# Kernel tuning notes

Hardware: AMD Instinct MI355X
Metric: run time of the kernel (lower is better)

Reference implementation:

```python
import jax, jax.numpy as jnp
import numpy as np

EPS = 1e-5  # torch LayerNorm default eps
L2_EPS = 1e-12


def _l2norm(t, axis=-1):
    return t / jnp.sqrt(jnp.sum(t * t, axis=axis, keepdims=True) + L2_EPS)


def setup_inputs() -> dict:
    key = jax.random.key(0)
    k1, k2, k3 = jax.random.split(key, 3)
    b, n, d = 4, 2048, 1024
    h, e, cs = 8, 16, 2048
    x = jax.random.normal(k1, (b, n, d), dtype=jnp.float32)
    # xavier_normal_ on [h, d, e]: fan_in = d*e, fan_out = h*e
    std = float(np.sqrt(2.0 / (d * e + h * e)))
    rand_projs = jax.random.normal(k2, (h, d, e), dtype=jnp.float32) * std
    codebook = jax.random.normal(k3, (h, cs, e), dtype=jnp.float32)
    return {"x": x, "rand_projs": rand_projs, "codebook": codebook}


def reference(x, rand_projs, codebook):
    # LayerNorm over last dim, no affine
    mu = jnp.mean(x, axis=-1, keepdims=True)
    var = jnp.mean((x - mu) ** 2, axis=-1, keepdims=True)
    xn = (x - mu) / jnp.sqrt(var + EPS)
    # per-head random projection: [b,n,d] x [h,d,e] -> [b,n,h,e]
    proj = jnp.einsum('bnd,hde->bnhe', xn, rand_projs)
    # cosine-sim VQ per head: normalize both, argmax similarity
    q = _l2norm(proj, axis=-1)                 # [b,n,h,e]
    cb = _l2norm(codebook, axis=-1)            # [h,c,e]
    sim = jnp.einsum('bnhe,hce->bnhc', q, cb)  # [b,n,h,c]
    indices = jnp.argmax(sim, axis=-1)         # [b,n,h] int
    return indices
```

## Files before the change

kernel.cpp:

```cpp
#include <hip/hip_runtime.h>
#include <math.h>


typedef short bf16x8 __attribute__((ext_vector_type(8)));
typedef float f32x4 __attribute__((ext_vector_type(4)));

__device__ __forceinline__ void stage16(const float* g, float* lds_base) {
  __builtin_amdgcn_global_load_lds(
      (const __attribute__((address_space(1))) void*)g,
      (__attribute__((address_space(3))) void*)lds_base, 16, 0, 0);
}

__device__ __forceinline__ unsigned short f2bf(float f) {
  unsigned u = __builtin_bit_cast(unsigned, f);
  unsigned r = (u + 0x7FFFu + ((u >> 16) & 1u)) >> 16;
  return (unsigned short)r;
}
__device__ __forceinline__ float bf2f(unsigned short b) {
  return __builtin_bit_cast(float, (unsigned)b << 16);
}
__device__ __forceinline__ void split3(float v, unsigned short& h,
                                       unsigned short& m, unsigned short& l) {
  h = f2bf(v);
  float r = v - bf2f(h);
  m = f2bf(r);
  float r2 = r - bf2f(m);
  l = f2bf(r2);
}

__global__ __launch_bounds__(256) void k_cbnorm(const float* __restrict__ cb,
                                                unsigned short* __restrict__ cfrag) {
  int v = blockIdx.x * 256 + threadIdx.x;
  int h = v >> 11, c = v & 2047, tl = c >> 4, n = c & 15;
  const float4* p = (const float4*)(cb + (size_t)v * 16);
  float4 q0 = p[0], q1 = p[1], q2 = p[2], q3 = p[3];
  float f[16] = {q0.x,q0.y,q0.z,q0.w, q1.x,q1.y,q1.z,q1.w,
                 q2.x,q2.y,q2.z,q2.w, q3.x,q3.y,q3.z,q3.w};
  double s = 0.0;
#pragma unroll
  for (int i = 0; i < 16; ++i) s += (double)f[i] * (double)f[i];
  double inv = 1.0 / sqrt(s + 1e-12);
  __attribute__((aligned(16))) unsigned short vp[3][16];
#pragma unroll
  for (int i = 0; i < 16; ++i)
    split3((float)((double)f[i] * inv), vp[0][i], vp[1][i], vp[2][i]);
#pragma unroll
  for (int pp = 0; pp < 3; ++pp) {
    size_t base = ((((size_t)h * 128 + tl) * 3 + pp) * 16 + n) * 16;
    ((bf16x8*)(cfrag + base))[0] = ((bf16x8*)vp[pp])[0];
    ((bf16x8*)(cfrag + base))[1] = ((bf16x8*)vp[pp])[1];
  }
}

__global__ __launch_bounds__(256) void k_colsum(const float* __restrict__ W,
                                                float* __restrict__ cs) {
  __shared__ float red[16][17];
  int h = blockIdx.x;
  int e = threadIdx.x & 15, part = threadIdx.x >> 4;
  const float* base = W + h * 16384 + e;
  float s = 0.f;
  int d0 = part * 64;
  for (int i = 0; i < 64; ++i) s += base[(d0 + i) * 16];
  red[e][part] = s;
  __syncthreads();
  if (threadIdx.x < 16) {
    float t = 0.f;
#pragma unroll
    for (int p = 0; p < 16; ++p) t += red[threadIdx.x][p];
    cs[h * 16 + threadIdx.x] = t;
  }
}

__global__ __launch_bounds__(256) void k_wsplit(const float* __restrict__ W,
                                                unsigned short* __restrict__ wfrag) {
  int id = blockIdx.x * 256 + threadIdx.x;
  int o = id & 1, n = (id >> 1) & 15, c = (id >> 5) & 7, dg = id >> 8;
  __attribute__((aligned(16))) unsigned short vp[3][8];
#pragma unroll
  for (int j = 0; j < 8; ++j) {
    float v = W[c * 16384 + (dg * 16 + o * 8 + j) * 16 + n];
    split3(v, vp[0][j], vp[1][j], vp[2][j]);
  }
#pragma unroll
  for (int pp = 0; pp < 3; ++pp) {
    size_t base = ((((size_t)dg * 8 + c) * 3 + pp) * 16 + n) * 16 + o * 8;
    *(bf16x8*)(wfrag + base) = *(bf16x8*)vp[pp];
  }
}

__global__ __launch_bounds__(256) void k_proj(const float* __restrict__ x,
                                              const unsigned short* __restrict__ wfrag,
                                              const float* __restrict__ csum,
                                              unsigned short* __restrict__ ph,
                                              unsigned short* __restrict__ pm,
                                              unsigned short* __restrict__ pl) {
  __shared__ float sAcc[4][64][33];
  __shared__ float sPs[4][2][16];
  __shared__ float sMu[16];
  const int t = threadIdx.x;
  const int lane = t & 63, w = t >> 6;
  const int r0 = blockIdx.x * 16;
  const int q = lane >> 4, n16 = lane & 15, oct = q & 1;
  const bool qlt2 = (q < 2);
  const int p1 = qlt2 ? 0 : 1, p2 = qlt2 ? 1 : 0, p3 = qlt2 ? 2 : 0;
  const int row = r0 + n16;

  f32x4 acc[8];
#pragma unroll
  for (int h = 0; h < 8; ++h) acc[h] = (f32x4){0.f, 0.f, 0.f, 0.f};
  float ps = 0.f;

  for (int dg2 = 0; dg2 < 16; ++dg2) {
    const int dg = w * 16 + dg2;
    const int dq = dg * 16 + oct * 8;
    float4 xa = *(const float4*)(x + (size_t)row * 1024 + dq);
    float4 xb = *(const float4*)(x + (size_t)row * 1024 + dq + 4);
    float xf[8] = {xa.x, xa.y, xa.z, xa.w, xb.x, xb.y, xb.z, xb.w};
    ps += ((xf[0] + xf[1]) + (xf[2] + xf[3])) +
          ((xf[4] + xf[5]) + (xf[6] + xf[7]));
    __attribute__((aligned(16))) unsigned short s1[8], s3[8];
#pragma unroll
    for (int j = 0; j < 8; ++j) {
      unsigned short hh, mm, ll;
      split3(xf[j], hh, mm, ll);
      s1[j] = qlt2 ? hh : mm;
      s3[j] = qlt2 ? hh : ll;
    }
    bf16x8 a1 = *(bf16x8*)s1;
    bf16x8 a3 = *(bf16x8*)s3;
#pragma unroll
    for (int hh = 0; hh < 8; ++hh) {
      size_t b0 = (((size_t)(dg * 8 + hh) * 3) * 16 + n16) * 16 + oct * 8;
      bf16x8 b1 = *(const bf16x8*)(wfrag + b0 + p1 * 256);
      bf16x8 b2 = *(const bf16x8*)(wfrag + b0 + p2 * 256);
      bf16x8 b3 = *(const bf16x8*)(wfrag + b0 + p3 * 256);
      acc[hh] = __builtin_amdgcn_mfma_f32_16x16x32_bf16(a1, b1, acc[hh], 0, 0, 0);
      acc[hh] = __builtin_amdgcn_mfma_f32_16x16x32_bf16(a1, b2, acc[hh], 0, 0, 0);
      acc[hh] = __builtin_amdgcn_mfma_f32_16x16x32_bf16(a3, b3, acc[hh], 0, 0, 0);
    }
  }

#pragma unroll
  for (int hh = 0; hh < 8; ++hh)
#pragma unroll
    for (int r = 0; r < 4; ++r) sAcc[w][lane][hh * 4 + r] = acc[hh][r];
  if (q < 2) sPs[w][q][n16] = ps;
  __syncthreads();
  if (t < 16) {
    float s = 0.f;
#pragma unroll
    for (int w2 = 0; w2 < 4; ++w2) s += sPs[w2][0][t] + sPs[w2][1][t];
    sMu[t] = s * (1.0f / 1024.0f);
  }
  __syncthreads();

  const int l = t & 63, g = t >> 6;
  const int lq = l >> 4, ln = l & 15;
#pragma unroll
  for (int hh2 = 0; hh2 < 2; ++hh2) {
    const int head = g * 2 + hh2;
    const float cs = csum[head * 16 + ln];
#pragma unroll
    for (int r = 0; r < 4; ++r) {
      const int f = head * 4 + r;
      float v = ((sAcc[0][l][f] + sAcc[1][l][f]) +
                 (sAcc[2][l][f] + sAcc[3][l][f]));
      const int row16 = lq * 4 + r;
      float tv = v - sMu[row16] * cs;
      unsigned short vh, vm, vl;
      split3(tv, vh, vm, vl);
      size_t base = ((size_t)head * 8192 + r0 + row16) * 16 + ln;
      ph[base] = vh; pm[base] = vm; pl[base] = vl;
    }
  }
}

__global__ __launch_bounds__(256) void k_argmax(
    const unsigned short* __restrict__ ph, const unsigned short* __restrict__ pm,
    const unsigned short* __restrict__ pl, const unsigned short* __restrict__ cfrag,
    float* __restrict__ amv, int* __restrict__ ami) {
  __shared__ __align__(16) unsigned short sB[12288];
  const int t = threadIdx.x;
  const int lane = t & 63, w = t >> 6;
  const int h = blockIdx.y;
  const int z = blockIdx.z;
  const int r0 = blockIdx.x * 256 + w * 64;
  const int q = lane >> 4, n16 = lane & 15;
  const int ehalf = (q & 1) * 8;
  const bool qlt2 = (q < 2);
  const int p1 = qlt2 ? 0 : 1, p2 = qlt2 ? 1 : 0, p3 = qlt2 ? 2 : 0;

  const float* src = (const float*)(cfrag + ((size_t)(h * 128 + z * 16) * 3) * 256);
#pragma unroll
  for (int i = 0; i < 6; ++i)
    stage16(src + ((size_t)((i * 4 + w) * 64) + lane) * 4,
            (float*)sB + (i * 4 + w) * 256);

  const unsigned short* pa1 = qlt2 ? ph : pm;
  const unsigned short* pa3 = qlt2 ? ph : pl;
  bf16x8 a1[4], a3[4];
#pragma unroll
  for (int rt = 0; rt < 4; ++rt) {
    size_t off = ((size_t)h * 8192 + r0 + rt * 16 + n16) * 16 + ehalf;
    a1[rt] = *(const bf16x8*)(pa1 + off);
    a3[rt] = *(const bf16x8*)(pa3 + off);
  }

  float best[4][4];
  int   bidx[4][4];
#pragma unroll
  for (int rt = 0; rt < 4; ++rt)
#pragma unroll
    for (int r = 0; r < 4; ++r) { best[rt][r] = -3.402823466e38f; bidx[rt][r] = 0; }

  __syncthreads();

  for (int tile = 0; tile < 16; ++tile) {
    const int b0 = tile * 768 + n16 * 16 + ehalf;
    bf16x8 b1 = *(const bf16x8*)(sB + b0 + p1 * 256);
    bf16x8 b2 = *(const bf16x8*)(sB + b0 + p2 * 256);
    bf16x8 b3 = *(const bf16x8*)(sB + b0 + p3 * 256);
    const int code = z * 256 + tile * 16 + n16;
#pragma unroll
    for (int rt = 0; rt < 4; ++rt) {
      f32x4 acc = {0.f, 0.f, 0.f, 0.f};
      acc = __builtin_amdgcn_mfma_f32_16x16x32_bf16(a1[rt], b1, acc, 0, 0, 0);
      acc = __builtin_amdgcn_mfma_f32_16x16x32_bf16(a1[rt], b2, acc, 0, 0, 0);
      acc = __builtin_amdgcn_mfma_f32_16x16x32_bf16(a3[rt], b3, acc, 0, 0, 0);
#pragma unroll
      for (int r = 0; r < 4; ++r)
        if (acc[r] > best[rt][r]) { best[rt][r] = acc[r]; bidx[rt][r] = code; }
    }
  }

#pragma unroll
  for (int off = 8; off >= 1; off >>= 1) {
#pragma unroll
    for (int rt = 0; rt < 4; ++rt)
#pragma unroll
      for (int r = 0; r < 4; ++r) {
        float ov = __shfl_xor(best[rt][r], off, 16);
        int   oi = __shfl_xor(bidx[rt][r], off, 16);
        if (ov > best[rt][r] || (ov == best[rt][r] && oi < bidx[rt][r])) {
          best[rt][r] = ov; bidx[rt][r] = oi;
        }
      }
  }
  if (n16 == 0) {
#pragma unroll
    for (int rt = 0; rt < 4; ++rt)
#pragma unroll
      for (int r = 0; r < 4; ++r) {
        int row = r0 + rt * 16 + q * 4 + r;
        size_t o = (size_t)z * 65536 + (size_t)row * 8 + h;
        amv[o] = best[rt][r]; ami[o] = bidx[rt][r];
      }
  }
}

__global__ __launch_bounds__(256) void k_amred(const float* __restrict__ amv,
                                               const int* __restrict__ ami,
                                               int* __restrict__ out) {
  int i = blockIdx.x * 256 + threadIdx.x;
  float bv = amv[i]; int bi = ami[i];
#pragma unroll
  for (int z = 1; z < 8; ++z) {
    float v = amv[(size_t)z * 65536 + i];
    if (v > bv) { bv = v; bi = ami[(size_t)z * 65536 + i]; }
  }
  out[i] = bi;
}

extern "C" void kernel_launch(void* const* d_in, const int* in_sizes, int n_in,
                              void* d_out, int out_size, void* d_ws, size_t ws_size,
                              hipStream_t stream) {
  (void)in_sizes; (void)n_in; (void)out_size; (void)ws_size;
  const float* x  = (const float*)d_in[0];
  const float* rp = (const float*)d_in[1];
  const float* cb = (const float*)d_in[2];
  int* out = (int*)d_out;

  float* ws = (float*)d_ws;
  float*          csum  = ws;
  float*          amv   = ws + 128;
  int*            ami   = (int*)(ws + 524416);
  unsigned short* wfrag = (unsigned short*)(ws + 1048704);
  unsigned short* cfrag = (unsigned short*)(ws + 1245312);
  unsigned short* ph    = (unsigned short*)(ws + 1638528);
  unsigned short* pm    = (unsigned short*)(ws + 2162816);
  unsigned short* pl    = (unsigned short*)(ws + 2687104);

  hipLaunchKernelGGL(k_cbnorm,  dim3(64),        dim3(256), 0, stream, cb, cfrag);
  hipLaunchKernelGGL(k_colsum,  dim3(8),         dim3(256), 0, stream, rp, csum);
  hipLaunchKernelGGL(k_wsplit,  dim3(64),        dim3(256), 0, stream, rp, wfrag);
  hipLaunchKernelGGL(k_proj,    dim3(512),       dim3(256), 0, stream, x, wfrag, csum, ph, pm, pl);
  hipLaunchKernelGGL(k_argmax,  dim3(32, 8, 8),  dim3(256), 0, stream, ph, pm, pl, cfrag, amv, ami);
  hipLaunchKernelGGL(k_amred,   dim3(256),       dim3(256), 0, stream, amv, ami, out);
}
```

Baseline: 161.1 us.

## Merge prep kernels into one launch and split projection K across eight waves

Measured after the change: 147.4 us. 1.09x faster.

```diff
diff --git a/kernel.cpp b/kernel.cpp
--- a/kernel.cpp
+++ b/kernel.cpp
@@ -28,74 +28,75 @@
   l = f2bf(r2);
 }
 
-__global__ __launch_bounds__(256) void k_cbnorm(const float* __restrict__ cb,
-                                                unsigned short* __restrict__ cfrag) {
-  int v = blockIdx.x * 256 + threadIdx.x;
-  int h = v >> 11, c = v & 2047, tl = c >> 4, n = c & 15;
-  const float4* p = (const float4*)(cb + (size_t)v * 16);
-  float4 q0 = p[0], q1 = p[1], q2 = p[2], q3 = p[3];
-  float f[16] = {q0.x,q0.y,q0.z,q0.w, q1.x,q1.y,q1.z,q1.w,
-                 q2.x,q2.y,q2.z,q2.w, q3.x,q3.y,q3.z,q3.w};
-  double s = 0.0;
-#pragma unroll
-  for (int i = 0; i < 16; ++i) s += (double)f[i] * (double)f[i];
-  double inv = 1.0 / sqrt(s + 1e-12);
-  __attribute__((aligned(16))) unsigned short vp[3][16];
-#pragma unroll
-  for (int i = 0; i < 16; ++i)
-    split3((float)((double)f[i] * inv), vp[0][i], vp[1][i], vp[2][i]);
-#pragma unroll
-  for (int pp = 0; pp < 3; ++pp) {
-    size_t base = ((((size_t)h * 128 + tl) * 3 + pp) * 16 + n) * 16;
-    ((bf16x8*)(cfrag + base))[0] = ((bf16x8*)vp[pp])[0];
-    ((bf16x8*)(cfrag + base))[1] = ((bf16x8*)vp[pp])[1];
-  }
-}
-
-__global__ __launch_bounds__(256) void k_colsum(const float* __restrict__ W,
-                                                float* __restrict__ cs) {
+__global__ __launch_bounds__(256) void k_prep(const float* __restrict__ cb,
+                                              const float* __restrict__ W,
+                                              unsigned short* __restrict__ cfrag,
+                                              float* __restrict__ csum,
+                                              unsigned short* __restrict__ wfrag) {
   __shared__ float red[16][17];
-  int h = blockIdx.x;
-  int e = threadIdx.x & 15, part = threadIdx.x >> 4;
-  const float* base = W + h * 16384 + e;
-  float s = 0.f;
-  int d0 = part * 64;
-  for (int i = 0; i < 64; ++i) s += base[(d0 + i) * 16];
-  red[e][part] = s;
-  __syncthreads();
-  if (threadIdx.x < 16) {
-    float t = 0.f;
-#pragma unroll
-    for (int p = 0; p < 16; ++p) t += red[threadIdx.x][p];
-    cs[h * 16 + threadIdx.x] = t;
-  }
-}
-
-__global__ __launch_bounds__(256) void k_wsplit(const float* __restrict__ W,
-                                                unsigned short* __restrict__ wfrag) {
-  int id = blockIdx.x * 256 + threadIdx.x;
-  int o = id & 1, n = (id >> 1) & 15, c = (id >> 5) & 7, dg = id >> 8;
-  __attribute__((aligned(16))) unsigned short vp[3][8];
-#pragma unroll
-  for (int j = 0; j < 8; ++j) {
-    float v = W[c * 16384 + (dg * 16 + o * 8 + j) * 16 + n];
-    split3(v, vp[0][j], vp[1][j], vp[2][j]);
-  }
-#pragma unroll
-  for (int pp = 0; pp < 3; ++pp) {
-    size_t base = ((((size_t)dg * 8 + c) * 3 + pp) * 16 + n) * 16 + o * 8;
-    *(bf16x8*)(wfrag + base) = *(bf16x8*)vp[pp];
-  }
-}
-
-__global__ __launch_bounds__(256) void k_proj(const float* __restrict__ x,
+  const int bid = blockIdx.x;
+  const int t = threadIdx.x;
+  if (bid < 64) {
+    int v = bid * 256 + t;
+    int h = v >> 11, c = v & 2047, tl = c >> 4, n = c & 15;
+    const float4* p = (const float4*)(cb + (size_t)v * 16);
+    float4 q0 = p[0], q1 = p[1], q2 = p[2], q3 = p[3];
+    float f[16] = {q0.x,q0.y,q0.z,q0.w, q1.x,q1.y,q1.z,q1.w,
+                   q2.x,q2.y,q2.z,q2.w, q3.x,q3.y,q3.z,q3.w};
+    double s = 0.0;
+#pragma unroll
+    for (int i = 0; i < 16; ++i) s += (double)f[i] * (double)f[i];
+    double inv = 1.0 / sqrt(s + 1e-12);
+    __attribute__((aligned(16))) unsigned short vp[3][16];
+#pragma unroll
+    for (int i = 0; i < 16; ++i)
+      split3((float)((double)f[i] * inv), vp[0][i], vp[1][i], vp[2][i]);
+#pragma unroll
+    for (int pp = 0; pp < 3; ++pp) {
+      size_t base = ((((size_t)h * 128 + tl) * 3 + pp) * 16 + n) * 16;
+      ((bf16x8*)(cfrag + base))[0] = ((bf16x8*)vp[pp])[0];
+      ((bf16x8*)(cfrag + base))[1] = ((bf16x8*)vp[pp])[1];
+    }
+  } else if (bid < 72) {
+    int h = bid - 64;
+    int e = t & 15, part = t >> 4;
+    const float* base = W + h * 16384 + e;
+    float s = 0.f;
+    int d0 = part * 64;
+    for (int i = 0; i < 64; ++i) s += base[(d0 + i) * 16];
+    red[e][part] = s;
+    __syncthreads();
+    if (t < 16) {
+      float tt = 0.f;
+#pragma unroll
+      for (int p = 0; p < 16; ++p) tt += red[t][p];
+      csum[h * 16 + t] = tt;
+    }
+  } else {
+    int id = (bid - 72) * 256 + t;
+    int o = id & 1, n = (id >> 1) & 15, c = (id >> 5) & 7, dg = id >> 8;
+    __attribute__((aligned(16))) unsigned short vp[3][8];
+#pragma unroll
+    for (int j = 0; j < 8; ++j) {
+      float v = W[c * 16384 + (dg * 16 + o * 8 + j) * 16 + n];
+      split3(v, vp[0][j], vp[1][j], vp[2][j]);
+    }
+#pragma unroll
+    for (int pp = 0; pp < 3; ++pp) {
+      size_t base = ((((size_t)dg * 8 + c) * 3 + pp) * 16 + n) * 16 + o * 8;
+      *(bf16x8*)(wfrag + base) = *(bf16x8*)vp[pp];
+    }
+  }
+}
+
+__global__ __launch_bounds__(512) void k_proj(const float* __restrict__ x,
                                               const unsigned short* __restrict__ wfrag,
                                               const float* __restrict__ csum,
                                               unsigned short* __restrict__ ph,
                                               unsigned short* __restrict__ pm,
                                               unsigned short* __restrict__ pl) {
   __shared__ float sAcc[4][64][33];
-  __shared__ float sPs[4][2][16];
+  __shared__ float sPs[8][2][16];
   __shared__ float sMu[16];
   const int t = threadIdx.x;
   const int lane = t & 63, w = t >> 6;
@@ -110,8 +111,9 @@
   for (int h = 0; h < 8; ++h) acc[h] = (f32x4){0.f, 0.f, 0.f, 0.f};
   float ps = 0.f;
 
-  for (int dg2 = 0; dg2 < 16; ++dg2) {
-    const int dg = w * 16 + dg2;
+#pragma unroll 4
+  for (int dg2 = 0; dg2 < 8; ++dg2) {
+    const int dg = w * 8 + dg2;
     const int dq = dg * 16 + oct * 8;
     float4 xa = *(const float4*)(x + (size_t)row * 1024 + dq);
     float4 xb = *(const float4*)(x + (size_t)row * 1024 + dq + 4);
@@ -140,38 +142,43 @@
     }
   }
 
-#pragma unroll
-  for (int hh = 0; hh < 8; ++hh)
-#pragma unroll
-    for (int r = 0; r < 4; ++r) sAcc[w][lane][hh * 4 + r] = acc[hh][r];
+  if (w >= 4) {
+#pragma unroll
+    for (int hh = 0; hh < 8; ++hh)
+#pragma unroll
+      for (int r = 0; r < 4; ++r) sAcc[w - 4][lane][hh * 4 + r] = acc[hh][r];
+  }
   if (q < 2) sPs[w][q][n16] = ps;
   __syncthreads();
+  if (w < 4) {
+#pragma unroll
+    for (int hh = 0; hh < 8; ++hh)
+#pragma unroll
+      for (int r = 0; r < 4; ++r)
+        sAcc[w][lane][hh * 4 + r] = acc[hh][r] + sAcc[w][lane][hh * 4 + r];
+  }
   if (t < 16) {
     float s = 0.f;
 #pragma unroll
-    for (int w2 = 0; w2 < 4; ++w2) s += sPs[w2][0][t] + sPs[w2][1][t];
+    for (int w2 = 0; w2 < 8; ++w2) s += sPs[w2][0][t] + sPs[w2][1][t];
     sMu[t] = s * (1.0f / 1024.0f);
   }
   __syncthreads();
 
-  const int l = t & 63, g = t >> 6;
+  const int l = t & 63, head = t >> 6;
   const int lq = l >> 4, ln = l & 15;
-#pragma unroll
-  for (int hh2 = 0; hh2 < 2; ++hh2) {
-    const int head = g * 2 + hh2;
-    const float cs = csum[head * 16 + ln];
-#pragma unroll
-    for (int r = 0; r < 4; ++r) {
-      const int f = head * 4 + r;
-      float v = ((sAcc[0][l][f] + sAcc[1][l][f]) +
-                 (sAcc[2][l][f] + sAcc[3][l][f]));
-      const int row16 = lq * 4 + r;
-      float tv = v - sMu[row16] * cs;
-      unsigned short vh, vm, vl;
-      split3(tv, vh, vm, vl);
-      size_t base = ((size_t)head * 8192 + r0 + row16) * 16 + ln;
-      ph[base] = vh; pm[base] = vm; pl[base] = vl;
-    }
+  const float cs = csum[head * 16 + ln];
+#pragma unroll
+  for (int r = 0; r < 4; ++r) {
+    const int f = head * 4 + r;
+    float v = ((sAcc[0][l][f] + sAcc[1][l][f]) +
+               (sAcc[2][l][f] + sAcc[3][l][f]));
+    const int row16 = lq * 4 + r;
+    float tv = v - sMu[row16] * cs;
+    unsigned short vh, vm, vl;
+    split3(tv, vh, vm, vl);
+    size_t base = ((size_t)head * 8192 + r0 + row16) * 16 + ln;
+    ph[base] = vh; pm[base] = vm; pl[base] = vl;
   }
 }
 
@@ -290,10 +297,8 @@
   unsigned short* pm    = (unsigned short*)(ws + 2162816);
   unsigned short* pl    = (unsigned short*)(ws + 2687104);
 
-  hipLaunchKernelGGL(k_cbnorm,  dim3(64),        dim3(256), 0, stream, cb, cfrag);
-  hipLaunchKernelGGL(k_colsum,  dim3(8),         dim3(256), 0, stream, rp, csum);
-  hipLaunchKernelGGL(k_wsplit,  dim3(64),        dim3(256), 0, stream, rp, wfrag);
-  hipLaunchKernelGGL(k_proj,    dim3(512),       dim3(256), 0, stream, x, wfrag, csum, ph, pm, pl);
+  hipLaunchKernelGGL(k_prep,    dim3(136),       dim3(256), 0, stream, cb, rp, cfrag, csum, wfrag);
+  hipLaunchKernelGGL(k_proj,    dim3(512),       dim3(512), 0, stream, x, wfrag, csum, ph, pm, pl);
   hipLaunchKernelGGL(k_argmax,  dim3(32, 8, 8),  dim3(256), 0, stream, ph, pm, pl, cfrag, amv, ami);
   hipLaunchKernelGGL(k_amred,   dim3(256),       dim3(256), 0, stream, amv, ami, out);
 }
```
